# Kernel tuning notes

Hardware: AMD Instinct MI355X
Metric: run time of the kernel (lower is better)

## Reference

```python
import jax, jax.numpy as jnp
import numpy as np

D_MODEL = 1024
EXPAND = 2
D_INNER = D_MODEL * EXPAND  # 2048
D_STATE = 16
DT_RANK = 64
CONV_K = 4
LN_EPS = 1e-5
B_SZ, SEQ = 2, 2048


def setup_inputs() -> dict:
    key = jax.random.key(0)
    ks = jax.random.split(key, 10)
    x = jax.random.normal(ks[0], (B_SZ, SEQ, D_MODEL), dtype=jnp.float32)
    ln_g = jnp.ones((D_MODEL,), jnp.float32)
    ln_b = jnp.zeros((D_MODEL,), jnp.float32)
    W_in = jax.random.normal(ks[1], (2 * D_INNER, D_MODEL), jnp.float32) * 0.02
    conv_w = jax.random.normal(ks[2], (D_INNER, 1, CONV_K), jnp.float32) * 0.2
    conv_b = jnp.zeros((D_INNER,), jnp.float32)
    # A_log = log(repeat(arange(1..d_state), d_inner))
    A_log = jnp.log(jnp.broadcast_to(jnp.arange(1, D_STATE + 1, dtype=jnp.float32), (D_INNER, D_STATE)))
    D_param = jnp.ones((D_INNER,), jnp.float32)
    x_proj_w = jax.random.normal(ks[3], (DT_RANK + 2 * D_STATE, D_INNER), jnp.float32) * 0.02
    dt_std = DT_RANK ** -0.5
    dt_w = jax.random.uniform(ks[4], (D_INNER, DT_RANK), jnp.float32, -dt_std, dt_std)
    dt = jnp.exp(jax.random.uniform(ks[5], (D_INNER,), jnp.float32) * (np.log(0.1) - np.log(0.001)) + np.log(0.001))
    dt_b = dt + jnp.log(-jnp.expm1(-dt))  # inverse softplus
    W_out = jax.random.normal(ks[6], (D_MODEL, D_INNER), jnp.float32) * 0.02
    return dict(x=x, ln_g=ln_g, ln_b=ln_b, W_in=W_in, conv_w=conv_w, conv_b=conv_b,
                A_log=A_log, D_param=D_param, x_proj_w=x_proj_w, dt_w=dt_w, dt_b=dt_b, W_out=W_out)


def _selective_scan(u, delta, A, B, C):
    # u, delta: (b,l,d); A: (d,n); B, C: (b,l,n)
    deltaA = jnp.exp(delta[..., None] * A[None, None])          # (b,l,d,n)
    dBu = delta[..., None] * B[:, :, None, :] * u[..., None]    # (b,l,d,n)

    def step(s, inp):
        dA_t, dBu_t, C_t = inp          # (b,d,n), (b,d,n), (b,n)
        s = dA_t * s + dBu_t
        y = jnp.einsum('bdn,bn->bd', s, C_t)
        return s, y

    s0 = jnp.zeros((u.shape[0], u.shape[2], A.shape[1]), u.dtype)
    xs = (jnp.moveaxis(deltaA, 1, 0), jnp.moveaxis(dBu, 1, 0), jnp.moveaxis(C, 1, 0))
    _, ys = jax.lax.scan(step, s0, xs)
    return jnp.moveaxis(ys, 0, 1)       # (b,l,d)


def reference(x, ln_g, ln_b, W_in, conv_w, conv_b, A_log, D_param, x_proj_w, dt_w, dt_b, W_out):
    residual = x
    mu = jnp.mean(x, -1, keepdims=True)
    var = jnp.var(x, -1, keepdims=True)
    xn = (x - mu) * jax.lax.rsqrt(var + LN_EPS) * ln_g + ln_b
    xz = xn @ W_in.T                               # (b,l,2*d_inner)
    xc, z = jnp.split(xz, 2, axis=-1)
    # causal depthwise conv1d (left-pad k-1)
    lhs = jnp.swapaxes(xc, 1, 2)                   # (b,d,l)
    conv = jax.lax.conv_general_dilated(
        lhs, conv_w, window_strides=(1,), padding=[(CONV_K - 1, 0)],
        dimension_numbers=('NCH', 'OIH', 'NCH'), feature_group_count=D_INNER)
    conv = conv + conv_b[None, :, None]
    xc = jax.nn.silu(jnp.swapaxes(conv, 1, 2))     # (b,l,d)
    # selective SSM
    x_dbl = xc @ x_proj_w.T
    delta_r, B, C = jnp.split(x_dbl, [DT_RANK, DT_RANK + D_STATE], axis=-1)
    delta = jax.nn.softplus(delta_r @ dt_w.T + dt_b)
    A = -jnp.exp(A_log)
    y = _selective_scan(xc, delta, A, B, C)
    y = y + xc * D_param
    y = y * jax.nn.silu(z)
    out = y @ W_out.T
    return out + residual
```

## Files before the change

### kernel.cpp

```cpp
#include <hip/hip_runtime.h>
#include <hip/hip_bf16.h>
#include <math.h>

typedef __hip_bfloat16 bf16;

#define D_MODEL 1024
#define D_INNER 2048
#define NTOK    4096
#define SEQ     2048
#define BSZ     2
#define DSTATE  16
#define DTRANK  64
#define NCH     64
#define CHLEN   32
#define NPAIR   4096
#define XDS     128

__device__ __forceinline__ float b2f(bf16 v) { return __bfloat162float(v); }
__device__ __forceinline__ bf16  f2b(float v) { return __float2bfloat16(v); }
__device__ __forceinline__ short f2bs(float v) {
    bf16 h = __float2bfloat16(v);
    short s; __builtin_memcpy(&s, &h, 2); return s;
}

typedef __attribute__((ext_vector_type(8))) short short8;
typedef __attribute__((ext_vector_type(4))) float f32x4;

__device__ __forceinline__ void async_copy16(const void* g, void* l) {
    __builtin_amdgcn_global_load_lds(
        (const __attribute__((address_space(1))) unsigned int*)g,
        (__attribute__((address_space(3))) unsigned int*)l,
        16, 0, 0);
}

__global__ void k_prep(const float* __restrict__ x, const float* __restrict__ g,
                       const float* __restrict__ b, bf16* __restrict__ xn,
                       const float* __restrict__ W_in, short* __restrict__ wInb,
                       const float* __restrict__ xpw, short* __restrict__ xpwb,
                       const float* __restrict__ dtw, short* __restrict__ dtwb,
                       float* __restrict__ xdbl) {
    int bid = blockIdx.x;
    int tid = threadIdx.x;
    if (bid < 4096) {
        int t = bid;
        const float* row = x + (size_t)t * D_MODEL;
        float v[4];
        float s = 0.f, q = 0.f;
#pragma unroll
        for (int i = 0; i < 4; ++i) {
            int idx = tid + i * 256;
            v[i] = row[idx];
            s += v[i]; q += v[i] * v[i];
        }
        __shared__ float sh_s[256], sh_q[256];
        sh_s[tid] = s; sh_q[tid] = q;
        __syncthreads();
        for (int o = 128; o > 0; o >>= 1) {
            if (tid < o) { sh_s[tid] += sh_s[tid + o]; sh_q[tid] += sh_q[tid + o]; }
            __syncthreads();
        }
        float mu  = sh_s[0] * (1.f / D_MODEL);
        float var = sh_q[0] * (1.f / D_MODEL) - mu * mu;
        float rs  = rsqrtf(var + 1e-5f);
#pragma unroll
        for (int i = 0; i < 4; ++i) {
            int idx = tid + i * 256;
            float o = (v[i] - mu) * rs * g[idx] + b[idx];
            xn[(size_t)t * D_MODEL + idx] = f2b(o);
        }
    } else if (bid < 8192) {
        int i = (bid - 4096) * 256 + tid;
        float4 v = reinterpret_cast<const float4*>(W_in)[i];
        short4 o;
        o.x = f2bs(v.x); o.y = f2bs(v.y); o.z = f2bs(v.z); o.w = f2bs(v.w);
        reinterpret_cast<short4*>(wInb)[i] = o;
    } else if (bid < 8448) {
        int i = (bid - 8192) * 256 + tid;
        int row = i >> 9;
        short4 o;
        if (row < 96) {
            float4 v = reinterpret_cast<const float4*>(xpw)[i];
            o.x = f2bs(v.x); o.y = f2bs(v.y); o.z = f2bs(v.z); o.w = f2bs(v.w);
        } else { o.x = o.y = o.z = o.w = 0; }
        reinterpret_cast<short4*>(xpwb)[i] = o;
    } else if (bid < 8576) {
        int i = (bid - 8448) * 256 + tid;
        float4 v = reinterpret_cast<const float4*>(dtw)[i];
        short4 o;
        o.x = f2bs(v.x); o.y = f2bs(v.y); o.z = f2bs(v.z); o.w = f2bs(v.w);
        reinterpret_cast<short4*>(dtwb)[i] = o;
    } else {
        int i = (bid - 8576) * 256 + tid;
        reinterpret_cast<float4*>(xdbl)[i] = (float4){0.f, 0.f, 0.f, 0.f};
    }
}

__global__ void k_f2b(const float* __restrict__ in, short* __restrict__ out) {
    int i = blockIdx.x * 256 + threadIdx.x;
    float4 v = reinterpret_cast<const float4*>(in)[i];
    short4 o;
    o.x = f2bs(v.x); o.y = f2bs(v.y); o.z = f2bs(v.z); o.w = f2bs(v.w);
    reinterpret_cast<short4*>(out)[i] = o;
}

__global__ void k_extract_dr(const float* __restrict__ xdbl, short* __restrict__ drb) {
    int i = blockIdx.x * 256 + threadIdx.x;
    int t = i >> 4;
    int jg = (i & 15) * 4;
    float4 v = *reinterpret_cast<const float4*>(&xdbl[(size_t)t * XDS + jg]);
    short4 o;
    o.x = f2bs(v.x); o.y = f2bs(v.y); o.z = f2bs(v.z); o.w = f2bs(v.w);
    *reinterpret_cast<short4*>(&drb[(size_t)t * DTRANK + jg]) = o;
}

#define GBK 32
template<int NT>
__global__ __launch_bounds__(256) void k_gemm_mfma(
    const short* __restrict__ A, const short* __restrict__ Bw,
    int N, int K, int mode,
    float* __restrict__ Cf, bf16* __restrict__ Cz,
    const float* __restrict__ res, float* __restrict__ Cout,
    const float* __restrict__ bias)
{
    constexpr int ABUF = 128 * GBK;
    constexpr int BBUF = NT * GBK;
    constexpr int AF   = (NT == 128) ? 4 : 2;
    __shared__ short As[2 * ABUF];
    __shared__ short Bs[2 * BBUF];
    const int tid  = threadIdx.x;
    const int lane = tid & 63;
    const int wave = tid >> 6;
    const int rowbase = (NT == 128) ? (wave >> 1) * 64 : wave * 32;
    const int colbase = (NT == 128) ? (wave & 1) * 64 : 0;
    const int m0 = blockIdx.y * 128;
    const int n0 = blockIdx.x * NT;
    const int lm = lane & 15;
    const int koff = (((lane >> 4) ^ ((lane >> 1) & 3)) * 8);

    const int srow = tid >> 2;
    const int skc  = (((tid & 3) ^ ((tid >> 3) & 3)) * 8);
    const size_t a_off0 = (size_t)(m0 + srow) * K + skc;
    const size_t a_off1 = (size_t)(m0 + srow + 64) * K + skc;
    const size_t b_off0 = (size_t)(n0 + srow) * K + skc;
    size_t b_off1 = 0;
    if constexpr (NT == 128) b_off1 = (size_t)(n0 + srow + 64) * K + skc;

    f32x4 acc[AF][4];
#pragma unroll
    for (int i = 0; i < AF; ++i)
#pragma unroll
        for (int j = 0; j < 4; ++j)
            acc[i][j] = (f32x4){0.f, 0.f, 0.f, 0.f};

    const int kchunk = K / gridDim.z;
    const int kbeg = blockIdx.z * kchunk;
    const int kend = kbeg + kchunk;

    {
        char* aD = (char*)As + tid * 16;
        char* bD = (char*)Bs + tid * 16;
        async_copy16(A + a_off0 + kbeg, aD);
        async_copy16(A + a_off1 + kbeg, aD + 4096);
        async_copy16(Bw + b_off0 + kbeg, bD);
        if constexpr (NT == 128) async_copy16(Bw + b_off1 + kbeg, bD + 4096);
    }

    int cur = 0;
    for (int k0 = kbeg; k0 < kend; k0 += GBK) {
        __syncthreads();
        int k1 = k0 + GBK;
        if (k1 < kend) {
            int nxt = cur ^ 1;
            char* aD = (char*)As + nxt * (ABUF * 2) + tid * 16;
            char* bD = (char*)Bs + nxt * (BBUF * 2) + tid * 16;
            async_copy16(A + a_off0 + k1, aD);
            async_copy16(A + a_off1 + k1, aD + 4096);
            async_copy16(Bw + b_off0 + k1, bD);
            if constexpr (NT == 128) async_copy16(Bw + b_off1 + k1, bD + 4096);
        }

        const short* Ab = As + cur * ABUF;
        const short* Bb = Bs + cur * BBUF;
        short8 af[AF], bf[4];
#pragma unroll
        for (int t = 0; t < AF; ++t)
            af[t] = *reinterpret_cast<const short8*>(&Ab[(rowbase + t * 16 + lm) * GBK + koff]);
#pragma unroll
        for (int t = 0; t < 4; ++t)
            bf[t] = *reinterpret_cast<const short8*>(&Bb[(colbase + t * 16 + lm) * GBK + koff]);
#pragma unroll
        for (int tm = 0; tm < AF; ++tm)
#pragma unroll
            for (int tn = 0; tn < 4; ++tn)
                acc[tm][tn] = __builtin_amdgcn_mfma_f32_16x16x32_bf16(
                    af[tm], bf[tn], acc[tm][tn], 0, 0, 0);
        cur ^= 1;
    }

    const int rq = (lane >> 4) * 4;
#pragma unroll
    for (int tm = 0; tm < AF; ++tm) {
#pragma unroll
        for (int tn = 0; tn < 4; ++tn) {
            f32x4 v = acc[tm][tn];
            int col = n0 + colbase + tn * 16 + lm;
#pragma unroll
            for (int r = 0; r < 4; ++r) {
                int row = m0 + rowbase + tm * 16 + rq + r;
                float val = v[r];
                if (mode == 0) {
                    if (col < D_INNER) Cf[(size_t)row * D_INNER + col] = val;
                    else               Cz[(size_t)row * D_INNER + (col - D_INNER)] = f2b(val);
                } else if (mode == 1) {
                    Cout[(size_t)row * N + col] = val + res[(size_t)row * N + col];
                } else if (mode == 2) {
                    atomicAdd(&Cf[(size_t)row * N + col], val);
                } else if (mode == 3) {
                    float a = val + bias[col];
                    float sp = (a > 20.f) ? a : log1pf(expf(a));
                    Cf[(size_t)row * N + col] = sp;
                } else {
                    Cf[(size_t)blockIdx.z * 4096 * N + (size_t)row * N + col] = val;
                }
            }
        }
    }
}

__global__ __launch_bounds__(512, 2) void k_gemm8(
    const short* __restrict__ A, const short* __restrict__ Bw,
    int N, int K, int mode,
    float* __restrict__ Cf, bf16* __restrict__ Cz)
{
    __shared__ short lds[65536];
    char* ldsc = (char*)lds;
    const int tid  = threadIdx.x;
    const int lane = tid & 63;
    const int wave = tid >> 6;
    const int wr   = wave >> 2;
    const int wc   = wave & 3;
    const int lm   = lane & 15;
    const int q4   = lane >> 4;
    const int m0 = blockIdx.y * 256;
    const int n0 = blockIdx.x * 256;

    const int r0  = tid >> 3;
    const int ksw = ((tid & 7) ^ (r0 & 7)) << 3;

    const int NTt   = K / 64 / gridDim.z;
    const int kbase = blockIdx.z * NTt;

    const short* gA = A  + (size_t)(m0 + r0) * K + ksw;
    const short* gB = Bw + (size_t)(n0 + r0) * K + ksw;

#define STAGE_A8(h, kt, bb) do {                                             \
        const short* s_ = gA + (size_t)(h) * 128 * K + (size_t)(kt) * 64;    \
        char* d_ = ldsc + (bb) * 32768 + (h) * 16384 + tid * 16;             \
        async_copy16(s_, d_);                                                \
        async_copy16(s_ + (size_t)64 * K, d_ + 8192);                        \
    } while (0)
#define STAGE_B8(h, kt, bb) do {                                             \
        const short* s_ = gB + (size_t)(h) * 128 * K + (size_t)(kt) * 64;    \
        char* d_ = ldsc + 65536 + (bb) * 32768 + (h) * 16384 + tid * 16;     \
        async_copy16(s_, d_);                                                \
        async_copy16(s_ + (size_t)64 * K, d_ + 8192);                        \
    } while (0)

    f32x4 acc[2][2][4][2];
#pragma unroll
    for (int a = 0; a < 2; ++a)
#pragma unroll
        for (int c = 0; c < 2; ++c)
#pragma unroll
            for (int t = 0; t < 4; ++t)
#pragma unroll
                for (int u = 0; u < 2; ++u)
                    acc[a][c][t][u] = (f32x4){0.f, 0.f, 0.f, 0.f};

    STAGE_B8(0, kbase + 0, 0); STAGE_B8(1, kbase + 0, 0);
    STAGE_A8(0, kbase + 0, 0); STAGE_A8(1, kbase + 0, 0);
    STAGE_B8(0, kbase + 1, 1); STAGE_B8(1, kbase + 1, 1);
    asm volatile("s_waitcnt vmcnt(4)" ::: "memory");
    __builtin_amdgcn_s_barrier();

    short8 af[4][2], bf0[2][2], bf1[2][2];

    for (int tt = 0; tt < NTt; ++tt) {
        const int b  = tt & 1;
        const int bn = b ^ 1;
        const short* lA = lds + b * 16384 + wr * 8192;
        const short* lB = lds + 32768 + b * 16384 + (wc >> 1) * 8192;
        const bool stA = (tt + 1 < NTt);
        const bool stB = (tt + 2 < NTt);

#pragma unroll
        for (int t = 0; t < 4; ++t) {
            const int rr = t * 16 + lm;
            const int x8 = rr & 7;
            af[t][0] = *reinterpret_cast<const short8*>(&lA[rr * 64 + ((q4 ^ x8) << 3)]);
            af[t][1] = *reinterpret_cast<const short8*>(&lA[rr * 64 + (((4 + q4) ^ x8) << 3)]);
        }
#pragma unroll
        for (int t = 0; t < 2; ++t) {
            const int rr = (wc & 1) * 64 + t * 16 + lm;
            const int x8 = rr & 7;
            bf0[t][0] = *reinterpret_cast<const short8*>(&lB[rr * 64 + ((q4 ^ x8) << 3)]);
            bf0[t][1] = *reinterpret_cast<const short8*>(&lB[rr * 64 + (((4 + q4) ^ x8) << 3)]);
        }
        if (stA) STAGE_A8(0, kbase + tt + 1, bn);
        __builtin_amdgcn_s_barrier();
        asm volatile("s_waitcnt lgkmcnt(0)" ::: "memory");
        __builtin_amdgcn_s_setprio(1);
#pragma unroll
        for (int t = 0; t < 4; ++t)
#pragma unroll
            for (int u = 0; u < 2; ++u) {
                acc[0][0][t][u] = __builtin_amdgcn_mfma_f32_16x16x32_bf16(af[t][0], bf0[u][0], acc[0][0][t][u], 0, 0, 0);
                acc[0][0][t][u] = __builtin_amdgcn_mfma_f32_16x16x32_bf16(af[t][1], bf0[u][1], acc[0][0][t][u], 0, 0, 0);
            }
        __builtin_amdgcn_s_setprio(0);
        __builtin_amdgcn_s_barrier();

#pragma unroll
        for (int t = 0; t < 2; ++t) {
            const int rr = (wc & 1) * 64 + 32 + t * 16 + lm;
            const int x8 = rr & 7;
            bf1[t][0] = *reinterpret_cast<const short8*>(&lB[rr * 64 + ((q4 ^ x8) << 3)]);
            bf1[t][1] = *reinterpret_cast<const short8*>(&lB[rr * 64 + (((4 + q4) ^ x8) << 3)]);
        }
        if (stA) STAGE_A8(1, kbase + tt + 1, bn);
        __builtin_amdgcn_s_barrier();
        asm volatile("s_waitcnt lgkmcnt(0)" ::: "memory");
        __builtin_amdgcn_s_setprio(1);
#pragma unroll
        for (int t = 0; t < 4; ++t)
#pragma unroll
            for (int u = 0; u < 2; ++u) {
                acc[0][1][t][u] = __builtin_amdgcn_mfma_f32_16x16x32_bf16(af[t][0], bf1[u][0], acc[0][1][t][u], 0, 0, 0);
                acc[0][1][t][u] = __builtin_amdgcn_mfma_f32_16x16x32_bf16(af[t][1], bf1[u][1], acc[0][1][t][u], 0, 0, 0);
            }
        __builtin_amdgcn_s_setprio(0);
        __builtin_amdgcn_s_barrier();

#pragma unroll
        for (int t = 0; t < 4; ++t) {
            const int rr = 64 + t * 16 + lm;
            const int x8 = rr & 7;
            af[t][0] = *reinterpret_cast<const short8*>(&lA[rr * 64 + ((q4 ^ x8) << 3)]);
            af[t][1] = *reinterpret_cast<const short8*>(&lA[rr * 64 + (((4 + q4) ^ x8) << 3)]);
        }
        if (stB) STAGE_B8(0, kbase + tt + 2, b);
        __builtin_amdgcn_s_barrier();
        asm volatile("s_waitcnt lgkmcnt(0)" ::: "memory");
        __builtin_amdgcn_s_setprio(1);
#pragma unroll
        for (int t = 0; t < 4; ++t)
#pragma unroll
            for (int u = 0; u < 2; ++u) {
                acc[1][1][t][u] = __builtin_amdgcn_mfma_f32_16x16x32_bf16(af[t][0], bf1[u][0], acc[1][1][t][u], 0, 0, 0);
                acc[1][1][t][u] = __builtin_amdgcn_mfma_f32_16x16x32_bf16(af[t][1], bf1[u][1], acc[1][1][t][u], 0, 0, 0);
            }
        __builtin_amdgcn_s_setprio(0);
        __builtin_amdgcn_s_barrier();

        if (stB) {
            STAGE_B8(1, kbase + tt + 2, b);
            asm volatile("s_waitcnt vmcnt(4)" ::: "memory");
        } else if (stA) {
            asm volatile("s_waitcnt vmcnt(0)" ::: "memory");
        }
        __builtin_amdgcn_s_barrier();
        __builtin_amdgcn_s_setprio(1);
#pragma unroll
        for (int t = 0; t < 4; ++t)
#pragma unroll
            for (int u = 0; u < 2; ++u) {
                acc[1][0][t][u] = __builtin_amdgcn_mfma_f32_16x16x32_bf16(af[t][0], bf0[u][0], acc[1][0][t][u], 0, 0, 0);
                acc[1][0][t][u] = __builtin_amdgcn_mfma_f32_16x16x32_bf16(af[t][1], bf0[u][1], acc[1][0][t][u], 0, 0, 0);
            }
        __builtin_amdgcn_s_setprio(0);
        __builtin_amdgcn_s_barrier();
    }
#undef STAGE_A8
#undef STAGE_B8

    const int rq = (lane >> 4) * 4;
#pragma unroll
    for (int qr = 0; qr < 2; ++qr)
#pragma unroll
    for (int qc = 0; qc < 2; ++qc)
#pragma unroll
    for (int t = 0; t < 4; ++t)
#pragma unroll
    for (int u = 0; u < 2; ++u) {
        f32x4 v = acc[qr][qc][t][u];
        const int col = n0 + wc * 64 + qc * 32 + u * 16 + lm;
#pragma unroll
        for (int r = 0; r < 4; ++r) {
            const int row = m0 + wr * 128 + qr * 64 + t * 16 + rq + r;
            if (mode == 0) {
                if (col < D_INNER) Cf[(size_t)row * D_INNER + col] = v[r];
                else               Cz[(size_t)row * D_INNER + (col - D_INNER)] = f2b(v[r]);
            } else {
                Cf[(size_t)blockIdx.z * 4096 * N + (size_t)row * N + col] = v[r];
            }
        }
    }
}

__global__ void k_reduce_out(const float* __restrict__ x, const float* __restrict__ P,
                             float* __restrict__ out) {
    int i = blockIdx.x * 256 + threadIdx.x;
    float4 a = reinterpret_cast<const float4*>(x)[i];
    float4 p = reinterpret_cast<const float4*>(P)[i];
    float4 q = reinterpret_cast<const float4*>(P + (size_t)4096 * 1024)[i];
    float4 o;
    o.x = a.x + p.x + q.x; o.y = a.y + p.y + q.y;
    o.z = a.z + p.z + q.z; o.w = a.w + p.w + q.w;
    reinterpret_cast<float4*>(out)[i] = o;
}

__global__ void k_conv(const float* __restrict__ xc, const float* __restrict__ cw,
                       const float* __restrict__ cb, bf16* __restrict__ xcs) {
    size_t idx = (size_t)blockIdx.x * blockDim.x + threadIdx.x;
    int d = (int)(idx & (D_INNER - 1));
    int l = (int)((idx >> 11) & (SEQ - 1));
    float w0 = cw[d * 4 + 0], w1 = cw[d * 4 + 1];
    float w2 = cw[d * 4 + 2], w3 = cw[d * 4 + 3];
    const float* base = xc + idx;
    float acc = cb[d] + w3 * base[0];
    if (l >= 1) acc += w2 * base[-(int)D_INNER];
    if (l >= 2) acc += w1 * base[-2 * (int)D_INNER];
    if (l >= 3) acc += w0 * base[-3 * (int)D_INNER];
    xcs[idx] = f2b(acc / (1.f + __expf(-acc)));
}

__global__ __launch_bounds__(256) void k_scan_partialB(
    const float* __restrict__ delta, const bf16* __restrict__ xcs,
    const float* __restrict__ xdbl, const float* __restrict__ A_log,
    bf16* __restrict__ chs, float* __restrict__ sumdl)
{
    __shared__ float Bsh[CHLEN][16];
    const int tid = threadIdx.x;
    const int d = blockIdx.x * 256 + tid;
    const int chunk = blockIdx.y;
    const int b = blockIdx.z;
    const size_t tbase = (size_t)b * SEQ + (size_t)chunk * CHLEN;

    if (tid < 128) {
        int t = tid >> 2, j = (tid & 3) * 4;
        float4 v = *reinterpret_cast<const float4*>(&xdbl[(tbase + t) * XDS + 64 + j]);
        *reinterpret_cast<float4*>(&Bsh[t][j]) = v;
    }
    float An[16];
#pragma unroll
    for (int j = 0; j < 4; ++j) {
        float4 v = *reinterpret_cast<const float4*>(&A_log[(size_t)d * DSTATE + j * 4]);
        An[j * 4 + 0] = -__expf(v.x); An[j * 4 + 1] = -__expf(v.y);
        An[j * 4 + 2] = -__expf(v.z); An[j * 4 + 3] = -__expf(v.w);
    }
    __syncthreads();

    float s[16];
#pragma unroll
    for (int n = 0; n < 16; ++n) s[n] = 0.f;
    float sd = 0.f;
    for (int t = 0; t < CHLEN; ++t) {
        size_t gt = tbase + t;
        float dl = delta[gt * D_INNER + d];
        float u  = b2f(xcs[gt * D_INNER + d]);
        float dlu = dl * u;
        sd += dl;
#pragma unroll
        for (int n = 0; n < 16; ++n) {
            float dA = __expf(dl * An[n]);
            s[n] = fmaf(dA, s[n], dlu * Bsh[t][n]);
        }
    }
    const int pair = b * D_INNER + d;
    bf16* co = chs + ((size_t)pair * NCH + chunk) * DSTATE;
#pragma unroll
    for (int n = 0; n < 16; ++n) co[n] = f2b(s[n]);
    sumdl[(size_t)pair * NCH + chunk] = sd;
}

__global__ void k_scan_combineB(const bf16* __restrict__ chs, const float* __restrict__ sumdl,
                                const float* __restrict__ A_log, bf16* __restrict__ sst) {
    int idx = blockIdx.x * 256 + threadIdx.x;
    int pair = idx >> 4;
    int n = idx & 15;
    int d = pair & (D_INNER - 1);
    float An = -__expf(A_log[(size_t)d * DSTATE + n]);
    float s = 0.f;
    for (int c = 0; c < NCH; ++c) {
        size_t o = ((size_t)pair * NCH + c) * DSTATE + n;
        float loc = b2f(chs[o]);
        float ap = __expf(An * sumdl[(size_t)pair * NCH + c]);
        sst[o] = f2b(s);
        s = fmaf(ap, s, loc);
    }
}

__global__ __launch_bounds__(256) void k_scan_finalB(
    const float* __restrict__ delta, const bf16* __restrict__ xcs,
    const float* __restrict__ xdbl, const bf16* __restrict__ zbuf,
    const float* __restrict__ A_log, const float* __restrict__ Dp,
    const bf16* __restrict__ sst, bf16* __restrict__ yf)
{
    __shared__ float BC[CHLEN][32];
    const int tid = threadIdx.x;
    const int d = blockIdx.x * 256 + tid;
    const int chunk = blockIdx.y;
    const int b = blockIdx.z;
    const size_t tbase = (size_t)b * SEQ + (size_t)chunk * CHLEN;

    {
        int t = tid >> 3, j = (tid & 7) * 4;
        float4 v = *reinterpret_cast<const float4*>(&xdbl[(tbase + t) * XDS + 64 + j]);
        *reinterpret_cast<float4*>(&BC[t][j]) = v;
    }
    float An[16];
#pragma unroll
    for (int j = 0; j < 4; ++j) {
        float4 v = *reinterpret_cast<const float4*>(&A_log[(size_t)d * DSTATE + j * 4]);
        An[j * 4 + 0] = -__expf(v.x); An[j * 4 + 1] = -__expf(v.y);
        An[j * 4 + 2] = -__expf(v.z); An[j * 4 + 3] = -__expf(v.w);
    }
    const int pair = b * D_INNER + d;
    float s[16];
    const bf16* so = sst + ((size_t)pair * NCH + chunk) * DSTATE;
#pragma unroll
    for (int n = 0; n < 16; ++n) s[n] = b2f(so[n]);
    const float Dv = Dp[d];
    __syncthreads();

    for (int t = 0; t < CHLEN; ++t) {
        size_t gt = tbase + t;
        float dl = delta[gt * D_INNER + d];
        float u  = b2f(xcs[gt * D_INNER + d]);
        float dlu = dl * u;
        float y = 0.f;
#pragma unroll
        for (int n = 0; n < 16; ++n) {
            float dA = __expf(dl * An[n]);
            s[n] = fmaf(dA, s[n], dlu * BC[t][n]);
            y = fmaf(s[n], BC[t][16 + n], y);
        }
        float zv = b2f(zbuf[gt * D_INNER + d]);
        float sz = zv / (1.f + __expf(-zv));
        yf[gt * D_INNER + d] = f2b((y + u * Dv) * sz);
    }
}

extern "C" void kernel_launch(void* const* d_in, const int* in_sizes, int n_in,
                              void* d_out, int out_size, void* d_ws, size_t ws_size,
                              hipStream_t stream) {
    const float* x      = (const float*)d_in[0];
    const float* ln_g   = (const float*)d_in[1];
    const float* ln_b   = (const float*)d_in[2];
    const float* W_in   = (const float*)d_in[3];
    const float* conv_w = (const float*)d_in[4];
    const float* conv_b = (const float*)d_in[5];
    const float* A_log  = (const float*)d_in[6];
    const float* D_par  = (const float*)d_in[7];
    const float* xpw    = (const float*)d_in[8];
    const float* dtw    = (const float*)d_in[9];
    const float* dtb    = (const float*)d_in[10];
    const float* W_out  = (const float*)d_in[11];
    float* out = (float*)d_out;

    char* ws = (char*)d_ws;
    bf16*  xn    = (bf16*)(ws + 0);
    bf16*  chs   = (bf16*)(ws + 0);
    bf16*  sst   = chs;
    short* wOutb = (short*)(ws + 0);
    float* xc    = (float*)(ws + 8388608);
    float* delta = xc;
    float* P0    = (float*)(ws + 8388608);
    bf16*  z     = (bf16*)(ws + 41943040);
    bf16*  yf    = z;
    short* wInb  = (short*)(ws + 58720256);
    bf16*  xcs   = (bf16*)(ws + 58720256);
    float* xdbl  = (float*)(ws + 75497472);
    float* sumdl = (float*)(ws + 77594624);
    short* drb   = (short*)(ws + 78643200);
    short* dtwb  = (short*)(ws + 79167488);
    short* xpwb  = (short*)(ws + 79429632);

    k_prep<<<9088, 256, 0, stream>>>(x, ln_g, ln_b, xn, W_in, wInb, xpw, xpwb, dtw, dtwb, xdbl);
    k_gemm8<<<dim3(4096 / 256, 4096 / 256, 1), 512, 0, stream>>>(
        (const short*)xn, wInb, 2 * D_INNER, D_MODEL, 0, xc, z);
    k_conv<<<(NTOK * D_INNER) / 256, 256, 0, stream>>>(xc, conv_w, conv_b, xcs);
    k_gemm_mfma<64><<<dim3(2, 32, 8), 256, 0, stream>>>(
        (const short*)xcs, xpwb, XDS, D_INNER, 2, xdbl, nullptr, nullptr, nullptr, nullptr);
    k_extract_dr<<<(NTOK * DTRANK / 4) / 256, 256, 0, stream>>>(xdbl, drb);
    k_gemm_mfma<64><<<dim3(D_INNER / 64, 32, 1), 256, 0, stream>>>(
        drb, dtwb, D_INNER, DTRANK, 3, delta, nullptr, nullptr, nullptr, dtb);
    k_scan_partialB<<<dim3(D_INNER / 256, NCH, BSZ), 256, 0, stream>>>(
        delta, xcs, xdbl, A_log, chs, sumdl);
    k_scan_combineB<<<(NPAIR * DSTATE) / 256, 256, 0, stream>>>(chs, sumdl, A_log, sst);
    k_scan_finalB<<<dim3(D_INNER / 256, NCH, BSZ), 256, 0, stream>>>(
        delta, xcs, xdbl, z, A_log, D_par, sst, yf);
    k_f2b<<<(D_MODEL * D_INNER / 4) / 256, 256, 0, stream>>>(W_out, wOutb);
    k_gemm8<<<dim3(D_MODEL / 256, 4096 / 256, 2), 512, 0, stream>>>(
        (const short*)yf, wOutb, D_MODEL, D_INNER, 4, P0, nullptr);
    k_reduce_out<<<(NTOK * D_MODEL / 4) / 256, 256, 0, stream>>>(x, P0, out);
}
```

Before: 373.9 us.

## Template GEMM M-tile and remap workgroups across XCDs for the output projection

The bf16 MFMA GEMM kernel is templated on the M-tile height (BM). The output projection now uses BM=128, which doubles its workgroup count so more of the device's compute units have work. Both GEMMs also get a workgroup index permutation that groups consecutive tiles per XCD, aiming for better L2 reuse. The smaller tile lowers per-block arithmetic intensity, and the async-copy wait counts now have to stay correct with fewer A copies in flight.

Result: faster. 363.2 us (-2.9%).

```diff
diff --git a/kernel.cpp b/kernel.cpp
--- a/kernel.cpp
+++ b/kernel.cpp
@@ -227,12 +227,18 @@
     }
 }
 
+template<int BM>
 __global__ __launch_bounds__(512, 2) void k_gemm8(
     const short* __restrict__ A, const short* __restrict__ Bw,
     int N, int K, int mode,
     float* __restrict__ Cf, bf16* __restrict__ Cz)
 {
-    __shared__ short lds[65536];
+    constexpr int WM    = BM / 2;
+    constexpr int MQ    = WM / 32;
+    constexpr int ATILE = BM * 64;
+    constexpr int ABYT  = BM * 128;
+    constexpr int BREG  = BM * 256;
+    __shared__ short lds[2 * ATILE + 2 * 16384];
     char* ldsc = (char*)lds;
     const int tid  = threadIdx.x;
     const int lane = tid & 63;
@@ -241,8 +247,13 @@
     const int wc   = wave & 3;
     const int lm   = lane & 15;
     const int q4   = lane >> 4;
-    const int m0 = blockIdx.y * 256;
-    const int n0 = blockIdx.x * 256;
+
+    const int gx = gridDim.x;
+    int n2 = blockIdx.y * gx + blockIdx.x;
+    const int nwg = gx * gridDim.y;
+    n2 = (n2 & 7) * (nwg >> 3) + (n2 >> 3);
+    const int m0 = (n2 / gx) * BM;
+    const int n0 = (n2 % gx) * 256;
 
     const int r0  = tid >> 3;
     const int ksw = ((tid & 7) ^ (r0 & 7)) << 3;
@@ -255,46 +266,47 @@
 
 #define STAGE_A8(h, kt, bb) do {                                             \
         const short* s_ = gA + (size_t)(h) * 128 * K + (size_t)(kt) * 64;    \
-        char* d_ = ldsc + (bb) * 32768 + (h) * 16384 + tid * 16;             \
+        char* d_ = ldsc + (bb) * ABYT + (h) * 16384 + tid * 16;              \
         async_copy16(s_, d_);                                                \
         async_copy16(s_ + (size_t)64 * K, d_ + 8192);                        \
     } while (0)
 #define STAGE_B8(h, kt, bb) do {                                             \
         const short* s_ = gB + (size_t)(h) * 128 * K + (size_t)(kt) * 64;    \
-        char* d_ = ldsc + 65536 + (bb) * 32768 + (h) * 16384 + tid * 16;     \
+        char* d_ = ldsc + BREG + (bb) * 32768 + (h) * 16384 + tid * 16;      \
         async_copy16(s_, d_);                                                \
         async_copy16(s_ + (size_t)64 * K, d_ + 8192);                        \
     } while (0)
 
-    f32x4 acc[2][2][4][2];
+    f32x4 acc[2][2][MQ][2];
 #pragma unroll
     for (int a = 0; a < 2; ++a)
 #pragma unroll
         for (int c = 0; c < 2; ++c)
 #pragma unroll
-            for (int t = 0; t < 4; ++t)
+            for (int t = 0; t < MQ; ++t)
 #pragma unroll
                 for (int u = 0; u < 2; ++u)
                     acc[a][c][t][u] = (f32x4){0.f, 0.f, 0.f, 0.f};
 
     STAGE_B8(0, kbase + 0, 0); STAGE_B8(1, kbase + 0, 0);
-    STAGE_A8(0, kbase + 0, 0); STAGE_A8(1, kbase + 0, 0);
+    STAGE_A8(0, kbase + 0, 0);
+    if constexpr (BM == 256) STAGE_A8(1, kbase + 0, 0);
     STAGE_B8(0, kbase + 1, 1); STAGE_B8(1, kbase + 1, 1);
     asm volatile("s_waitcnt vmcnt(4)" ::: "memory");
     __builtin_amdgcn_s_barrier();
 
-    short8 af[4][2], bf0[2][2], bf1[2][2];
+    short8 af[MQ][2], bf0[2][2], bf1[2][2];
 
     for (int tt = 0; tt < NTt; ++tt) {
         const int b  = tt & 1;
         const int bn = b ^ 1;
-        const short* lA = lds + b * 16384 + wr * 8192;
-        const short* lB = lds + 32768 + b * 16384 + (wc >> 1) * 8192;
+        const short* lA = lds + b * ATILE + wr * (WM * 64);
+        const short* lB = lds + BM * 128 + b * 16384 + (wc >> 1) * 8192;
         const bool stA = (tt + 1 < NTt);
         const bool stB = (tt + 2 < NTt);
 
 #pragma unroll
-        for (int t = 0; t < 4; ++t) {
+        for (int t = 0; t < MQ; ++t) {
             const int rr = t * 16 + lm;
             const int x8 = rr & 7;
             af[t][0] = *reinterpret_cast<const short8*>(&lA[rr * 64 + ((q4 ^ x8) << 3)]);
@@ -312,7 +324,7 @@
         asm volatile("s_waitcnt lgkmcnt(0)" ::: "memory");
         __builtin_amdgcn_s_setprio(1);
 #pragma unroll
-        for (int t = 0; t < 4; ++t)
+        for (int t = 0; t < MQ; ++t)
 #pragma unroll
             for (int u = 0; u < 2; ++u) {
                 acc[0][0][t][u] = __builtin_amdgcn_mfma_f32_16x16x32_bf16(af[t][0], bf0[u][0], acc[0][0][t][u], 0, 0, 0);
@@ -328,12 +340,12 @@
             bf1[t][0] = *reinterpret_cast<const short8*>(&lB[rr * 64 + ((q4 ^ x8) << 3)]);
             bf1[t][1] = *reinterpret_cast<const short8*>(&lB[rr * 64 + (((4 + q4) ^ x8) << 3)]);
         }
-        if (stA) STAGE_A8(1, kbase + tt + 1, bn);
+        if constexpr (BM == 256) { if (stA) STAGE_A8(1, kbase + tt + 1, bn); }
         __builtin_amdgcn_s_barrier();
         asm volatile("s_waitcnt lgkmcnt(0)" ::: "memory");
         __builtin_amdgcn_s_setprio(1);
 #pragma unroll
-        for (int t = 0; t < 4; ++t)
+        for (int t = 0; t < MQ; ++t)
 #pragma unroll
             for (int u = 0; u < 2; ++u) {
                 acc[0][1][t][u] = __builtin_amdgcn_mfma_f32_16x16x32_bf16(af[t][0], bf1[u][0], acc[0][1][t][u], 0, 0, 0);
@@ -343,8 +355,8 @@
         __builtin_amdgcn_s_barrier();
 
 #pragma unroll
-        for (int t = 0; t < 4; ++t) {
-            const int rr = 64 + t * 16 + lm;
+        for (int t = 0; t < MQ; ++t) {
+            const int rr = MQ * 16 + t * 16 + lm;
             const int x8 = rr & 7;
             af[t][0] = *reinterpret_cast<const short8*>(&lA[rr * 64 + ((q4 ^ x8) << 3)]);
             af[t][1] = *reinterpret_cast<const short8*>(&lA[rr * 64 + (((4 + q4) ^ x8) << 3)]);
@@ -354,7 +366,7 @@
         asm volatile("s_waitcnt lgkmcnt(0)" ::: "memory");
         __builtin_amdgcn_s_setprio(1);
 #pragma unroll
-        for (int t = 0; t < 4; ++t)
+        for (int t = 0; t < MQ; ++t)
 #pragma unroll
             for (int u = 0; u < 2; ++u) {
                 acc[1][1][t][u] = __builtin_amdgcn_mfma_f32_16x16x32_bf16(af[t][0], bf1[u][0], acc[1][1][t][u], 0, 0, 0);
@@ -372,7 +384,7 @@
         __builtin_amdgcn_s_barrier();
         __builtin_amdgcn_s_setprio(1);
 #pragma unroll
-        for (int t = 0; t < 4; ++t)
+        for (int t = 0; t < MQ; ++t)
 #pragma unroll
             for (int u = 0; u < 2; ++u) {
                 acc[1][0][t][u] = __builtin_amdgcn_mfma_f32_16x16x32_bf16(af[t][0], bf0[u][0], acc[1][0][t][u], 0, 0, 0);
@@ -390,14 +402,14 @@
 #pragma unroll
     for (int qc = 0; qc < 2; ++qc)
 #pragma unroll
-    for (int t = 0; t < 4; ++t)
+    for (int t = 0; t < MQ; ++t)
 #pragma unroll
     for (int u = 0; u < 2; ++u) {
         f32x4 v = acc[qr][qc][t][u];
         const int col = n0 + wc * 64 + qc * 32 + u * 16 + lm;
 #pragma unroll
         for (int r = 0; r < 4; ++r) {
-            const int row = m0 + wr * 128 + qr * 64 + t * 16 + rq + r;
+            const int row = m0 + wr * WM + qr * (WM / 2) + t * 16 + rq + r;
             if (mode == 0) {
                 if (col < D_INNER) Cf[(size_t)row * D_INNER + col] = v[r];
                 else               Cz[(size_t)row * D_INNER + (col - D_INNER)] = f2b(v[r]);
@@ -588,7 +600,7 @@
     short* xpwb  = (short*)(ws + 79429632);
 
     k_prep<<<9088, 256, 0, stream>>>(x, ln_g, ln_b, xn, W_in, wInb, xpw, xpwb, dtw, dtwb, xdbl);
-    k_gemm8<<<dim3(4096 / 256, 4096 / 256, 1), 512, 0, stream>>>(
+    k_gemm8<256><<<dim3(4096 / 256, 4096 / 256, 1), 512, 0, stream>>>(
         (const short*)xn, wInb, 2 * D_INNER, D_MODEL, 0, xc, z);
     k_conv<<<(NTOK * D_INNER) / 256, 256, 0, stream>>>(xc, conv_w, conv_b, xcs);
     k_gemm_mfma<64><<<dim3(2, 32, 8), 256, 0, stream>>>(
@@ -602,7 +614,7 @@
     k_scan_finalB<<<dim3(D_INNER / 256, NCH, BSZ), 256, 0, stream>>>(
         delta, xcs, xdbl, z, A_log, D_par, sst, yf);
     k_f2b<<<(D_MODEL * D_INNER / 4) / 256, 256, 0, stream>>>(W_out, wOutb);
-    k_gemm8<<<dim3(D_MODEL / 256, 4096 / 256, 2), 512, 0, stream>>>(
+    k_gemm8<128><<<dim3(D_MODEL / 256, 4096 / 128, 2), 512, 0, stream>>>(
         (const short*)yf, wOutb, D_MODEL, D_INNER, 4, P0, nullptr);
     k_reduce_out<<<(NTOK * D_MODEL / 4) / 256, 256, 0, stream>>>(x, P0, out);
 }
```
